# Optimization experiments

Measured on AMD Instinct MI355X. Metric: run time of the kernel, lower is better.

## Reference

```python
import jax, jax.numpy as jnp
import numpy as np

B, N, R = 64, 2000, 64
EMBED, LABELS = 512, 20
GRAPH_DIM = 1  # feature is unsqueezed to [B, N, 1]


def setup_inputs() -> dict:
    key = jax.random.key(0)
    ks = jax.random.split(key, 10)
    s = 0.05
    return {
        "feature": jax.random.normal(ks[0], (B, N), dtype=jnp.float32),
        "init_graph": jax.random.uniform(ks[1], (N, N), dtype=jnp.float32),
        "theta_w": jax.random.normal(ks[2], (R, GRAPH_DIM), dtype=jnp.float32) * s,
        "theta_b": jax.random.normal(ks[3], (R,), dtype=jnp.float32) * s,
        "phi_w": jax.random.normal(ks[4], (R, GRAPH_DIM), dtype=jnp.float32) * s,
        "phi_b": jax.random.normal(ks[5], (R,), dtype=jnp.float32) * s,
        "fc1_w": jax.random.normal(ks[6], (EMBED, N), dtype=jnp.float32) * s,
        "fc1_b": jax.random.normal(ks[7], (EMBED,), dtype=jnp.float32) * s,
        "fc2_w": jax.random.normal(ks[8], (LABELS, EMBED), dtype=jnp.float32) * s,
        "fc2_b": jax.random.normal(ks[9], (LABELS,), dtype=jnp.float32) * s,
    }


def reference(feature, init_graph, theta_w, theta_b, phi_w, phi_b,
              fc1_w, fc1_b, fc2_w, fc2_b):
    # graph_feature: [B, N, 1]; Linear(1, R) => f * w[:, 0] + b
    theta_f = feature[..., None] * theta_w[:, 0] + theta_b  # [B, N, R]
    phi_f = feature[..., None] * phi_w[:, 0] + phi_b        # [B, N, R]
    # similarity: [B, N, N], scaled by sqrt(graph_dim)=1
    sim = jnp.einsum('bnr,bmr->bnm', theta_f, phi_f) / np.sqrt(GRAPH_DIM)
    relation_graph = jax.nn.softmax(sim, axis=2)            # [B, N, N]
    # (init_graph + relation_graph) @ graph_feature -> [B, N]
    relation_feature = jax.nn.relu(
        jnp.einsum('bnm,bm->bn', init_graph[None] + relation_graph, feature))
    mixed = relation_feature + feature                      # [B, N] (dropout is eval-mode identity)
    hidden = jnp.tanh(mixed @ fc1_w.T + fc1_b)              # [B, EMBED]
    logits = hidden @ fc2_w.T + fc2_b                       # [B, LABELS]
    return logits
```

## Files before the change

kernel.cpp:

```cpp
#include <hip/hip_runtime.h>
#include <math.h>

#define B 64
#define N 2000
#define R 64
#define EMBED 512
#define LABELS 20

#define NM 23
#define NK 22

#define KS 25
#define KC 80
#define NT_GF 32
#define NT_FC 8

#define SC_OFF 0
#define S_OFF 64
#define FT_OFF 2048
#define MIX_OFF (FT_OFF + N * B)
#define HID_OFF (MIX_OFF + N * B)
#define PGF_OFF (HID_OFF + EMBED * B)
#define PFC_OFF (PGF_OFF + KS * N * B)

__constant__ float c_invfact[NK] = {
    1.0f, 1.0f, 0.5f,
    1.6666666666666666e-01f, 4.1666666666666664e-02f, 8.3333333333333332e-03f,
    1.3888888888888889e-03f, 1.9841269841269841e-04f, 2.4801587301587302e-05f,
    2.7557319223985893e-06f, 2.7557319223985894e-07f, 2.5052108385441720e-08f,
    2.0876756987868100e-09f, 1.6059043836821616e-10f, 1.1470745597729726e-11f,
    7.6471637318198170e-13f, 4.7794773323873860e-14f, 2.8114572543455206e-15f,
    1.5619206968586225e-16f, 8.2206352466243300e-18f, 4.1103176233121650e-19f,
    1.9572941063391263e-20f,
};

__global__ __launch_bounds__(256) void prep_fused(const float* __restrict__ f,
                                                  const float* __restrict__ tw,
                                                  const float* __restrict__ tb,
                                                  const float* __restrict__ pw,
                                                  float* __restrict__ sc,
                                                  float* __restrict__ S,
                                                  float* __restrict__ fT) {
    __shared__ float tile[64][65];
    __shared__ double sred[4][NM];
    int bid = blockIdx.x;
    int tid = threadIdx.x;
    if (bid >= 65) {
        int m0 = (bid - 65) * 64;
        int lane = tid & 63, w = tid >> 6;
        for (int bb = w; bb < 64; bb += 4)
            tile[lane][bb] = (m0 + lane < N) ? f[(size_t)bb * N + m0 + lane] : 0.f;
        __syncthreads();
        for (int mm = w; mm < 64; mm += 4)
            if (m0 + mm < N) fT[(size_t)(m0 + mm) * 64 + lane] = tile[mm][lane];
        return;
    }
    if (bid == 64) {
        if (tid < R) {
            float a = tw[tid] * pw[tid];
            float c = tb[tid] * pw[tid];
            for (int off = 32; off; off >>= 1) {
                a += __shfl_down(a, off);
                c += __shfl_down(c, off);
            }
            if (tid == 0) { sc[0] = a; sc[1] = c; }
        }
        return;
    }
    const float* fb = f + (size_t)bid * N;
    double acc[NM];
#pragma unroll
    for (int k = 0; k < NM; ++k) acc[k] = 0.0;
    for (int m = tid; m < N; m += 256) {
        double x = (double)fb[m];
        double p = 1.0;
#pragma unroll
        for (int k = 0; k < NM; ++k) { acc[k] += p; p *= x; }
    }
    for (int off = 32; off; off >>= 1) {
#pragma unroll
        for (int k = 0; k < NM; ++k) acc[k] += __shfl_down(acc[k], off);
    }
    int w = tid >> 6, lane = tid & 63;
    if (lane == 0) {
#pragma unroll
        for (int k = 0; k < NM; ++k) sred[w][k] = acc[k];
    }
    __syncthreads();
    if (tid < NM) {
        double s = sred[0][tid] + sred[1][tid] + sred[2][tid] + sred[3][tid];
        S[tid * 64 + bid] = (float)s;
    }
}

template <int M>
__global__ __launch_bounds__(512) void gemm_part(const float* __restrict__ A,
                                                 const float* __restrict__ X,
                                                 float* __restrict__ P) {
    int tid = threadIdx.x;
    int lane = tid & 63;
    int w = __builtin_amdgcn_readfirstlane(tid >> 6);
    int ks = blockIdx.x % KS;
    int nt = blockIdx.x / KS;
    int k0 = ks * KC;
    int row0 = nt * 64 + w * 8;

    float vf[KC];
#pragma unroll
    for (int j = 0; j < KC; ++j) vf[j] = X[(size_t)(k0 + j) * 64 + lane];

    int rowc[8];
#pragma unroll
    for (int r = 0; r < 8; ++r) rowc[r] = (row0 + r < M) ? (row0 + r) : (M - 1);

    float acc[8];
#pragma unroll
    for (int r = 0; r < 8; ++r) acc[r] = 0.f;

#pragma unroll
    for (int j4 = 0; j4 < KC / 4; ++j4) {
#pragma unroll
        for (int r = 0; r < 8; ++r) {
            const float4 g = *(const float4*)(A + (size_t)rowc[r] * N + k0 + 4 * j4);
            acc[r] = fmaf(g.x, vf[4 * j4 + 0], acc[r]);
            acc[r] = fmaf(g.y, vf[4 * j4 + 1], acc[r]);
            acc[r] = fmaf(g.z, vf[4 * j4 + 2], acc[r]);
            acc[r] = fmaf(g.w, vf[4 * j4 + 3], acc[r]);
        }
    }
#pragma unroll
    for (int r = 0; r < 8; ++r) {
        int row = row0 + r;
        if (row < M) P[((size_t)ks * M + row) * 64 + lane] = acc[r];
    }
}

__global__ __launch_bounds__(256) void reduce_gf(const float* __restrict__ P,
                                                 const float* __restrict__ fT,
                                                 const float* __restrict__ sc,
                                                 const float* __restrict__ S,
                                                 float* __restrict__ mixT) {
    int flat = blockIdx.x * 256 + threadIdx.x;
    int b = flat & 63;
    float s = 0.f;
#pragma unroll
    for (int k = 0; k < KS; ++k) s += P[(size_t)k * N * 64 + flat];
    float fn = fT[flat];
    float A = sc[0], C2 = sc[1];
    float t = fmaf(A, fn, C2);
    float Z = 0.f, Wv = 0.f, tp = 1.f;
#pragma unroll
    for (int k = 0; k < NK; ++k) {
        float c = tp * c_invfact[k];
        Z = fmaf(c, S[k * 64 + b], Z);
        Wv = fmaf(c, S[(k + 1) * 64 + b], Wv);
        tp *= t;
    }
    float r = fmaxf(s + Wv / Z, 0.f);
    mixT[flat] = r + fn;
}

__global__ __launch_bounds__(256) void reduce_fc1(const float* __restrict__ P,
                                                  const float* __restrict__ b1,
                                                  float* __restrict__ hidden) {
    int flat = blockIdx.x * 256 + threadIdx.x;
    int e = flat >> 6;
    float s = 0.f;
#pragma unroll
    for (int k = 0; k < KS; ++k) s += P[(size_t)k * EMBED * 64 + flat];
    hidden[flat] = tanhf(s + b1[e]);
}

__global__ __launch_bounds__(256) void fc2_kernel(const float* __restrict__ hidden,
                                                  const float* __restrict__ w2,
                                                  const float* __restrict__ b2,
                                                  float* __restrict__ out) {
    int l = blockIdx.x;
    int tid = threadIdx.x;
    int lane = tid & 63;
    int w = tid >> 6;
    const float4* W = (const float4*)(w2 + (size_t)l * EMBED) + w * 32;
    const float* h = hidden + (size_t)(w * 128) * B + lane;
    float a0 = 0.f, a1 = 0.f, a2 = 0.f, a3 = 0.f;
#pragma unroll 4
    for (int i = 0; i < 32; ++i) {
        float4 g = W[i];
        a0 = fmaf(g.x, h[(4 * i + 0) * B], a0);
        a1 = fmaf(g.y, h[(4 * i + 1) * B], a1);
        a2 = fmaf(g.z, h[(4 * i + 2) * B], a2);
        a3 = fmaf(g.w, h[(4 * i + 3) * B], a3);
    }
    __shared__ float part[4][64];
    part[w][lane] = (a0 + a1) + (a2 + a3);
    __syncthreads();
    if (w == 0) {
        out[(size_t)lane * LABELS + l] =
            part[0][lane] + part[1][lane] + part[2][lane] + part[3][lane] + b2[l];
    }
}

extern "C" void kernel_launch(void* const* d_in, const int* in_sizes, int n_in,
                              void* d_out, int out_size, void* d_ws, size_t ws_size,
                              hipStream_t stream) {
    const float* feature = (const float*)d_in[0];
    const float* init_graph = (const float*)d_in[1];
    const float* theta_w = (const float*)d_in[2];
    const float* theta_b = (const float*)d_in[3];
    const float* phi_w = (const float*)d_in[4];
    const float* fc1_w = (const float*)d_in[6];
    const float* fc1_b = (const float*)d_in[7];
    const float* fc2_w = (const float*)d_in[8];
    const float* fc2_b = (const float*)d_in[9];
    float* out = (float*)d_out;

    float* ws = (float*)d_ws;
    float* sc = ws + SC_OFF;
    float* S = ws + S_OFF;
    float* fT = ws + FT_OFF;
    float* mixT = ws + MIX_OFF;
    float* hidden = ws + HID_OFF;
    float* Pgf = ws + PGF_OFF;
    float* Pfc = ws + PFC_OFF;

    hipLaunchKernelGGL(prep_fused, dim3(65 + (N + 63) / 64), dim3(256), 0, stream,
                       feature, theta_w, theta_b, phi_w, sc, S, fT);
    hipLaunchKernelGGL((gemm_part<N>), dim3(NT_GF * KS), dim3(512), 0, stream,
                       init_graph, fT, Pgf);
    hipLaunchKernelGGL(reduce_gf, dim3(N * B / 256), dim3(256), 0, stream,
                       Pgf, fT, sc, S, mixT);
    hipLaunchKernelGGL((gemm_part<EMBED>), dim3(NT_FC * KS), dim3(512), 0, stream,
                       fc1_w, mixT, Pfc);
    hipLaunchKernelGGL(reduce_fc1, dim3(EMBED * B / 256), dim3(256), 0, stream,
                       Pfc, fc1_b, hidden);
    hipLaunchKernelGGL(fc2_kernel, dim3(LABELS), dim3(256), 0, stream,
                       hidden, fc2_w, fc2_b, out);
}
```

Baseline: 125.1 us.

## Fuse all stages into one cooperative persistent kernel with grid syncs

Replaces six separate kernel launches with a single cooperative kernel of 256 blocks that uses grid-wide syncs between the prep, graph GEMM, graph reduction, fc1 GEMM, fc1 reduction and fc2 stages. The GEMM now stages the X tile in XOR-swizzled shared memory instead of holding it in registers, and the split-K factors change (8 splits for the graph GEMM, 32 for fc1). The aim is to remove launch overhead and inter-kernel gaps. In exchange it adds grid-sync cost and runs the large graph GEMM with only 256 blocks, which may underuse the GPU's bandwidth.

```diff
diff --git a/kernel.cpp b/kernel.cpp
--- a/kernel.cpp
+++ b/kernel.cpp
@@ -1,19 +1,20 @@
 #include <hip/hip_runtime.h>
+#include <hip/hip_cooperative_groups.h>
 #include <math.h>
 
+namespace cg = cooperative_groups;
+
+#define N 2000
 #define B 64
-#define N 2000
-#define R 64
 #define EMBED 512
 #define LABELS 20
-
 #define NM 23
 #define NK 22
 
-#define KS 25
-#define KC 80
-#define NT_GF 32
-#define NT_FC 8
+#define GF_KS 8
+#define GF_KC 256
+#define FC_KS 32
+#define FC_KC 64
 
 #define SC_OFF 0
 #define S_OFF 64
@@ -21,7 +22,7 @@
 #define MIX_OFF (FT_OFF + N * B)
 #define HID_OFF (MIX_OFF + N * B)
 #define PGF_OFF (HID_OFF + EMBED * B)
-#define PFC_OFF (PGF_OFF + KS * N * B)
+#define PFC_OFF (PGF_OFF + GF_KS * N * B)
 
 __constant__ float c_invfact[NK] = {
     1.0f, 1.0f, 0.5f,
@@ -34,29 +35,118 @@
     1.9572941063391263e-20f,
 };
 
-__global__ __launch_bounds__(256) void prep_fused(const float* __restrict__ f,
-                                                  const float* __restrict__ tw,
-                                                  const float* __restrict__ tb,
-                                                  const float* __restrict__ pw,
-                                                  float* __restrict__ sc,
-                                                  float* __restrict__ S,
-                                                  float* __restrict__ fT) {
-    __shared__ float tile[64][65];
-    __shared__ double sred[4][NM];
+union SmemU {
+    float xsT[64 * GF_KC];
+    struct {
+        float tile[64][65];
+        double sred[8][NM];
+    } p0;
+    float part[8][64];
+};
+
+template <int KC>
+__device__ __forceinline__ void gemm_item(const float* __restrict__ A, int M,
+                                          const float* __restrict__ X,
+                                          float* __restrict__ P,
+                                          int nt, int ks, float* xsT, int tid) {
+    const int XORM = KC / 4 - 1;
+    int lane = tid & 63;
+    int w = __builtin_amdgcn_readfirstlane(tid >> 6);
+    int k0 = ks * KC;
+    for (int i = tid; i < 64 * KC; i += 512) {
+        int kk = i >> 6, b = i & 63;
+        float v = (k0 + kk < N) ? X[(size_t)(k0 + kk) * 64 + b] : 0.f;
+        xsT[b * KC + 4 * ((kk >> 2) ^ (b & XORM)) + (kk & 3)] = v;
+    }
+    __syncthreads();
+    int row0 = nt * 64 + w * 8;
+    int rowc[8];
+#pragma unroll
+    for (int r = 0; r < 8; ++r) rowc[r] = (row0 + r < M) ? (row0 + r) : (M - 1);
+    float acc[8];
+#pragma unroll
+    for (int r = 0; r < 8; ++r) acc[r] = 0.f;
+    int lx = lane & XORM;
+    const float* xrow = xsT + lane * KC;
+#pragma unroll 2
+    for (int k4 = 0; k4 < KC / 4; ++k4) {
+        int kb = k0 + 4 * k4;
+        int kbc = (kb + 3 < N) ? kb : (N - 4);
+        float4 xv = *(const float4*)(xrow + 4 * (k4 ^ lx));
+#pragma unroll
+        for (int r = 0; r < 8; ++r) {
+            float4 g = *(const float4*)(A + (size_t)rowc[r] * N + kbc);
+            acc[r] = fmaf(g.x, xv.x, acc[r]);
+            acc[r] = fmaf(g.y, xv.y, acc[r]);
+            acc[r] = fmaf(g.z, xv.z, acc[r]);
+            acc[r] = fmaf(g.w, xv.w, acc[r]);
+        }
+    }
+#pragma unroll
+    for (int r = 0; r < 8; ++r) {
+        int row = row0 + r;
+        if (row < M) P[((size_t)ks * M + row) * 64 + lane] = acc[r];
+    }
+    __syncthreads();
+}
+
+__global__ __launch_bounds__(512) void mega_kernel(
+        const float* __restrict__ f, const float* __restrict__ G,
+        const float* __restrict__ tw, const float* __restrict__ tb,
+        const float* __restrict__ pw,
+        const float* __restrict__ w1, const float* __restrict__ b1,
+        const float* __restrict__ w2, const float* __restrict__ b2,
+        float* __restrict__ out, float* __restrict__ ws) {
+    __shared__ SmemU sm;
+    cg::grid_group grid = cg::this_grid();
     int bid = blockIdx.x;
     int tid = threadIdx.x;
-    if (bid >= 65) {
-        int m0 = (bid - 65) * 64;
-        int lane = tid & 63, w = tid >> 6;
-        for (int bb = w; bb < 64; bb += 4)
-            tile[lane][bb] = (m0 + lane < N) ? f[(size_t)bb * N + m0 + lane] : 0.f;
+    int lane = tid & 63, w = tid >> 6;
+
+    float* sc = ws + SC_OFF;
+    float* S = ws + S_OFF;
+    float* fT = ws + FT_OFF;
+    float* mixT = ws + MIX_OFF;
+    float* hidden = ws + HID_OFF;
+    float* Pgf = ws + PGF_OFF;
+    float* Pfc = ws + PFC_OFF;
+
+    if (bid < 32) {
+        int m0 = bid * 64;
+        for (int bb = w; bb < 64; bb += 8)
+            sm.p0.tile[lane][bb] = (m0 + lane < N) ? f[(size_t)bb * N + m0 + lane] : 0.f;
         __syncthreads();
-        for (int mm = w; mm < 64; mm += 4)
-            if (m0 + mm < N) fT[(size_t)(m0 + mm) * 64 + lane] = tile[mm][lane];
-        return;
-    }
-    if (bid == 64) {
-        if (tid < R) {
+        for (int mm = w; mm < 64; mm += 8)
+            if (m0 + mm < N) fT[(size_t)(m0 + mm) * 64 + lane] = sm.p0.tile[mm][lane];
+    } else if (bid < 96) {
+        int b = bid - 32;
+        const float* fb = f + (size_t)b * N;
+        double acc[NM];
+#pragma unroll
+        for (int k = 0; k < NM; ++k) acc[k] = 0.0;
+        for (int m = tid; m < N; m += 512) {
+            double x = (double)fb[m];
+            double p = 1.0;
+#pragma unroll
+            for (int k = 0; k < NM; ++k) { acc[k] += p; p *= x; }
+        }
+        for (int off = 32; off; off >>= 1) {
+#pragma unroll
+            for (int k = 0; k < NM; ++k) acc[k] += __shfl_down(acc[k], off);
+        }
+        if (lane == 0) {
+#pragma unroll
+            for (int k = 0; k < NM; ++k) sm.p0.sred[w][k] = acc[k];
+        }
+        __syncthreads();
+        if (tid < NM) {
+            double s = 0.0;
+#pragma unroll
+            for (int ww = 0; ww < 8; ++ww) s += sm.p0.sred[ww][tid];
+            S[tid * 64 + b] = (float)s;
+        }
+    } else if (bid == 96) {
+        if (tid < 64) {
             float a = tw[tid] * pw[tid];
             float c = tb[tid] * pw[tid];
             for (int off = 32; off; off >>= 1) {
@@ -65,173 +155,89 @@
             }
             if (tid == 0) { sc[0] = a; sc[1] = c; }
         }
-        return;
-    }
-    const float* fb = f + (size_t)bid * N;
-    double acc[NM];
-#pragma unroll
-    for (int k = 0; k < NM; ++k) acc[k] = 0.0;
-    for (int m = tid; m < N; m += 256) {
-        double x = (double)fb[m];
-        double p = 1.0;
-#pragma unroll
-        for (int k = 0; k < NM; ++k) { acc[k] += p; p *= x; }
-    }
-    for (int off = 32; off; off >>= 1) {
-#pragma unroll
-        for (int k = 0; k < NM; ++k) acc[k] += __shfl_down(acc[k], off);
-    }
-    int w = tid >> 6, lane = tid & 63;
-    if (lane == 0) {
-#pragma unroll
-        for (int k = 0; k < NM; ++k) sred[w][k] = acc[k];
-    }
-    __syncthreads();
-    if (tid < NM) {
-        double s = sred[0][tid] + sred[1][tid] + sred[2][tid] + sred[3][tid];
-        S[tid * 64 + bid] = (float)s;
-    }
-}
-
-template <int M>
-__global__ __launch_bounds__(512) void gemm_part(const float* __restrict__ A,
-                                                 const float* __restrict__ X,
-                                                 float* __restrict__ P) {
-    int tid = threadIdx.x;
-    int lane = tid & 63;
-    int w = __builtin_amdgcn_readfirstlane(tid >> 6);
-    int ks = blockIdx.x % KS;
-    int nt = blockIdx.x / KS;
-    int k0 = ks * KC;
-    int row0 = nt * 64 + w * 8;
-
-    float vf[KC];
-#pragma unroll
-    for (int j = 0; j < KC; ++j) vf[j] = X[(size_t)(k0 + j) * 64 + lane];
-
-    int rowc[8];
-#pragma unroll
-    for (int r = 0; r < 8; ++r) rowc[r] = (row0 + r < M) ? (row0 + r) : (M - 1);
-
-    float acc[8];
-#pragma unroll
-    for (int r = 0; r < 8; ++r) acc[r] = 0.f;
-
-#pragma unroll
-    for (int j4 = 0; j4 < KC / 4; ++j4) {
-#pragma unroll
-        for (int r = 0; r < 8; ++r) {
-            const float4 g = *(const float4*)(A + (size_t)rowc[r] * N + k0 + 4 * j4);
-            acc[r] = fmaf(g.x, vf[4 * j4 + 0], acc[r]);
-            acc[r] = fmaf(g.y, vf[4 * j4 + 1], acc[r]);
-            acc[r] = fmaf(g.z, vf[4 * j4 + 2], acc[r]);
-            acc[r] = fmaf(g.w, vf[4 * j4 + 3], acc[r]);
-        }
-    }
-#pragma unroll
-    for (int r = 0; r < 8; ++r) {
-        int row = row0 + r;
-        if (row < M) P[((size_t)ks * M + row) * 64 + lane] = acc[r];
-    }
-}
-
-__global__ __launch_bounds__(256) void reduce_gf(const float* __restrict__ P,
-                                                 const float* __restrict__ fT,
-                                                 const float* __restrict__ sc,
-                                                 const float* __restrict__ S,
-                                                 float* __restrict__ mixT) {
-    int flat = blockIdx.x * 256 + threadIdx.x;
-    int b = flat & 63;
-    float s = 0.f;
-#pragma unroll
-    for (int k = 0; k < KS; ++k) s += P[(size_t)k * N * 64 + flat];
-    float fn = fT[flat];
-    float A = sc[0], C2 = sc[1];
-    float t = fmaf(A, fn, C2);
-    float Z = 0.f, Wv = 0.f, tp = 1.f;
-#pragma unroll
-    for (int k = 0; k < NK; ++k) {
-        float c = tp * c_invfact[k];
-        Z = fmaf(c, S[k * 64 + b], Z);
-        Wv = fmaf(c, S[(k + 1) * 64 + b], Wv);
-        tp *= t;
-    }
-    float r = fmaxf(s + Wv / Z, 0.f);
-    mixT[flat] = r + fn;
-}
-
-__global__ __launch_bounds__(256) void reduce_fc1(const float* __restrict__ P,
-                                                  const float* __restrict__ b1,
-                                                  float* __restrict__ hidden) {
-    int flat = blockIdx.x * 256 + threadIdx.x;
-    int e = flat >> 6;
-    float s = 0.f;
-#pragma unroll
-    for (int k = 0; k < KS; ++k) s += P[(size_t)k * EMBED * 64 + flat];
-    hidden[flat] = tanhf(s + b1[e]);
-}
-
-__global__ __launch_bounds__(256) void fc2_kernel(const float* __restrict__ hidden,
-                                                  const float* __restrict__ w2,
-                                                  const float* __restrict__ b2,
-                                                  float* __restrict__ out) {
-    int l = blockIdx.x;
-    int tid = threadIdx.x;
-    int lane = tid & 63;
-    int w = tid >> 6;
-    const float4* W = (const float4*)(w2 + (size_t)l * EMBED) + w * 32;
-    const float* h = hidden + (size_t)(w * 128) * B + lane;
-    float a0 = 0.f, a1 = 0.f, a2 = 0.f, a3 = 0.f;
-#pragma unroll 4
-    for (int i = 0; i < 32; ++i) {
-        float4 g = W[i];
-        a0 = fmaf(g.x, h[(4 * i + 0) * B], a0);
-        a1 = fmaf(g.y, h[(4 * i + 1) * B], a1);
-        a2 = fmaf(g.z, h[(4 * i + 2) * B], a2);
-        a3 = fmaf(g.w, h[(4 * i + 3) * B], a3);
-    }
-    __shared__ float part[4][64];
-    part[w][lane] = (a0 + a1) + (a2 + a3);
-    __syncthreads();
-    if (w == 0) {
-        out[(size_t)lane * LABELS + l] =
-            part[0][lane] + part[1][lane] + part[2][lane] + part[3][lane] + b2[l];
+    }
+    grid.sync();
+
+    gemm_item<GF_KC>(G, N, fT, Pgf, bid >> 3, bid & 7, sm.xsT, tid);
+    grid.sync();
+
+    {
+        int flat = bid * 512 + tid;
+        if (flat < N * 64) {
+            int b = flat & 63;
+            float s = 0.f;
+#pragma unroll
+            for (int k = 0; k < GF_KS; ++k) s += Pgf[(size_t)k * N * 64 + flat];
+            float fn = fT[flat];
+            float Ax = sc[0], C2 = sc[1];
+            float t = fmaf(Ax, fn, C2);
+            float Z = 0.f, Wv = 0.f, tp = 1.f;
+#pragma unroll
+            for (int k = 0; k < NK; ++k) {
+                float c = tp * c_invfact[k];
+                Z = fmaf(c, S[k * 64 + b], Z);
+                Wv = fmaf(c, S[(k + 1) * 64 + b], Wv);
+                tp *= t;
+            }
+            float r = fmaxf(s + Wv / Z, 0.f);
+            mixT[flat] = r + fn;
+        }
+    }
+    grid.sync();
+
+    gemm_item<FC_KC>(w1, EMBED, mixT, Pfc, bid >> 5, bid & 31, sm.xsT, tid);
+    grid.sync();
+
+    {
+        int flat = bid * 512 + tid;
+        if (flat < EMBED * 64) {
+            int e = flat >> 6;
+            float s = 0.f;
+#pragma unroll
+            for (int k = 0; k < FC_KS; ++k) s += Pfc[(size_t)k * EMBED * 64 + flat];
+            hidden[flat] = tanhf(s + b1[e]);
+        }
+    }
+    grid.sync();
+
+    if (bid < LABELS) {
+        int l = bid;
+        const float* h = hidden + (size_t)(w * 64) * 64 + lane;
+        const float* wr = w2 + (size_t)l * EMBED + w * 64;
+        float a0 = 0.f, a1 = 0.f;
+#pragma unroll
+        for (int i = 0; i < 64; i += 2) {
+            a0 = fmaf(wr[i], h[(size_t)i * 64], a0);
+            a1 = fmaf(wr[i + 1], h[(size_t)(i + 1) * 64], a1);
+        }
+        sm.part[w][lane] = a0 + a1;
+        __syncthreads();
+        if (w == 0) {
+            float s = 0.f;
+#pragma unroll
+            for (int ww = 0; ww < 8; ++ww) s += sm.part[ww][lane];
+            out[(size_t)lane * LABELS + l] = s + b2[l];
+        }
     }
 }
 
 extern "C" void kernel_launch(void* const* d_in, const int* in_sizes, int n_in,
                               void* d_out, int out_size, void* d_ws, size_t ws_size,
                               hipStream_t stream) {
-    const float* feature = (const float*)d_in[0];
-    const float* init_graph = (const float*)d_in[1];
-    const float* theta_w = (const float*)d_in[2];
-    const float* theta_b = (const float*)d_in[3];
-    const float* phi_w = (const float*)d_in[4];
-    const float* fc1_w = (const float*)d_in[6];
-    const float* fc1_b = (const float*)d_in[7];
-    const float* fc2_w = (const float*)d_in[8];
-    const float* fc2_b = (const float*)d_in[9];
+    const float* f = (const float*)d_in[0];
+    const float* G = (const float*)d_in[1];
+    const float* tw = (const float*)d_in[2];
+    const float* tb = (const float*)d_in[3];
+    const float* pw = (const float*)d_in[4];
+    const float* w1 = (const float*)d_in[6];
+    const float* b1 = (const float*)d_in[7];
+    const float* w2 = (const float*)d_in[8];
+    const float* b2 = (const float*)d_in[9];
     float* out = (float*)d_out;
-
-    float* ws = (float*)d_ws;
-    float* sc = ws + SC_OFF;
-    float* S = ws + S_OFF;
-    float* fT = ws + FT_OFF;
-    float* mixT = ws + MIX_OFF;
-    float* hidden = ws + HID_OFF;
-    float* Pgf = ws + PGF_OFF;
-    float* Pfc = ws + PFC_OFF;
-
-    hipLaunchKernelGGL(prep_fused, dim3(65 + (N + 63) / 64), dim3(256), 0, stream,
-                       feature, theta_w, theta_b, phi_w, sc, S, fT);
-    hipLaunchKernelGGL((gemm_part<N>), dim3(NT_GF * KS), dim3(512), 0, stream,
-                       init_graph, fT, Pgf);
-    hipLaunchKernelGGL(reduce_gf, dim3(N * B / 256), dim3(256), 0, stream,
-                       Pgf, fT, sc, S, mixT);
-    hipLaunchKernelGGL((gemm_part<EMBED>), dim3(NT_FC * KS), dim3(512), 0, stream,
-                       fc1_w, mixT, Pfc);
-    hipLaunchKernelGGL(reduce_fc1, dim3(EMBED * B / 256), dim3(256), 0, stream,
-                       Pfc, fc1_b, hidden);
-    hipLaunchKernelGGL(fc2_kernel, dim3(LABELS), dim3(256), 0, stream,
-                       hidden, fc2_w, fc2_b, out);
+    float* wsp = (float*)d_ws;
+
+    void* args[] = {(void*)&f, (void*)&G, (void*)&tw, (void*)&tb, (void*)&pw,
+                    (void*)&w1, (void*)&b1, (void*)&w2, (void*)&b2,
+                    (void*)&out, (void*)&wsp};
+    hipLaunchCooperativeKernel(mega_kernel, dim3(256), dim3(512), args, 0u, stream);
 }
```

After: 309.5 us. +147.5%, slower.
